# Optimization experiments

Hardware: AMD Instinct MI355X
Metric: run time of the kernel (lower is better)

The kernel has to match this reference:

```python
import jax, jax.numpy as jnp
import numpy as np

B, S, E, H = 16, 2048, 128, 128  # batch, seq_len, n_embd, head_dim


def setup_inputs() -> dict:
    key = jax.random.key(0)
    ks = jax.random.split(key, 6)
    init_s = 1.0 / np.sqrt(E)  # ~ torch Linear default init scale
    return {
        "q": jax.random.normal(ks[0], (B, S, E), jnp.float32),
        "k": jax.random.normal(ks[1], (B, S, E), jnp.float32),
        "v": jax.random.normal(ks[2], (B, S, E), jnp.float32),
        "Wq": jax.random.normal(ks[3], (H, E), jnp.float32) * init_s,
        "bq": jnp.zeros((H,), jnp.float32),
        "Wk": jax.random.normal(ks[4], (H, E), jnp.float32) * init_s,
        "bk": jnp.zeros((H,), jnp.float32),
        "Wv": jax.random.normal(ks[5], (H, E), jnp.float32) * init_s,
        "bv": jnp.zeros((H,), jnp.float32),
        "mask": jnp.tril(jnp.ones((S, S), jnp.float32)),  # causal mask
    }


def reference(q, k, v, Wq, bq, Wk, bk, Wv, bv, mask):
    # Linear projections: y = x @ W.T + b (torch nn.Linear convention)
    qh = q @ Wq.T + bq  # [B,S,H]
    kh = k @ Wk.T + bk  # [B,S,H]
    vh = v @ Wv.T + bv  # [B,S,H]
    d_k = kh.shape[-1]
    wei = jnp.einsum("bqd,bkd->bqk", qh, kh) * (d_k ** -0.5)  # [B,S,S]
    wei = jnp.where(mask == 0, -jnp.inf, wei)  # masked_fill(mask==0, -inf)
    attn = jax.nn.softmax(wei, axis=-1)
    return jnp.einsum("bqk,bkd->bqd", attn, vh)  # [B,S,H]
```

## Files before the change

### kernel.cpp

```cpp
#include <hip/hip_runtime.h>
#include <hip/hip_bf16.h>

#define BATCH 16
#define SEQ   2048
#define HD    128
#define TB    64
#define QB3   64
#define NT3   (SEQ/QB3)
#define PLANE ((size_t)BATCH*SEQ*HD)

typedef __attribute__((ext_vector_type(8))) short bf16x8;
typedef __attribute__((ext_vector_type(4))) float f32x4;
typedef __attribute__((ext_vector_type(2))) unsigned int u32x2;

#define MFMA(a,b,c) __builtin_amdgcn_mfma_f32_16x16x32_bf16(a,b,c,0,0,0)

__device__ __forceinline__ short f2bf(float f){
  union{float f; unsigned u;} v; v.f = f;
  unsigned r = (v.u + 0x7FFFu + ((v.u>>16)&1u))>>16;
  return (short)r;
}
__device__ __forceinline__ unsigned packbf(float lo, float hi){
  return ((unsigned)(unsigned short)f2bf(hi) << 16) | (unsigned short)f2bf(lo);
}
__device__ __forceinline__ bf16x8 pack8(f32x4 a, f32x4 b){
  bf16x8 r;
  r[0]=f2bf(a[0]); r[1]=f2bf(a[1]); r[2]=f2bf(a[2]); r[3]=f2bf(a[3]);
  r[4]=f2bf(b[0]); r[5]=f2bf(b[1]); r[6]=f2bf(b[2]); r[7]=f2bf(b[3]);
  return r;
}
__device__ __forceinline__ bf16x8 ldfrag(const float* base, size_t eo){
  const float* p = base + eo;
  return pack8(*(const f32x4*)p, *(const f32x4*)(p+4));
}

__global__ __launch_bounds__(256)
void wconv_kernel(const float* __restrict__ Wq, const float* __restrict__ Wk,
                  const float* __restrict__ Wv, short* __restrict__ wb)
{
  int i = (blockIdx.x*256 + threadIdx.x)*8;
  const float* src = (i < 16384) ? Wq : (i < 32768 ? Wk : Wv);
  int off = i & 16383;
  f32x4 a = *(const f32x4*)(src + off);
  f32x4 b = *(const f32x4*)(src + off + 4);
  *(bf16x8*)(wb + i) = pack8(a, b);
}

__global__ __launch_bounds__(256)
void proj_kernel(const float* __restrict__ k, const float* __restrict__ v,
                 const float* __restrict__ bk, const float* __restrict__ bv,
                 const short* __restrict__ wb, short* __restrict__ ws)
{
  __shared__ __align__(16) short T[TB*136];
  __shared__ __align__(16) short VT[HD*72];

  const int z = blockIdx.y + 1;
  const float* x  = (z==1) ? k  : v;
  const float* bb = (z==1) ? bk : bv;
  const short* W  = wb + (size_t)z*HD*HD;

  const int tid = threadIdx.x;
  const int w = tid>>6, l = tid&63, li = l&15, g = l>>4;
  const int bx = blockIdx.x;
  const int rowbase = bx*TB + w*16;

  bf16x8 afr[4];
  const float* xr = x + (size_t)(rowbase+li)*HD + g*8;
  #pragma unroll
  for (int ks=0; ks<4; ks++) afr[ks] = ldfrag(xr, (size_t)ks*32);

  f32x4 acc[8];
  #pragma unroll
  for (int ct=0; ct<8; ct++) acc[ct] = (f32x4){0.f,0.f,0.f,0.f};
  #pragma unroll
  for (int ct=0; ct<8; ct++){
    #pragma unroll
    for (int ks=0; ks<4; ks++){
      bf16x8 bfr = *(const bf16x8*)(W + (size_t)(ct*16+li)*HD + ks*32 + g*8);
      acc[ct] = MFMA(afr[ks], bfr, acc[ct]);
    }
  }

  const int img  = (bx>>1);
  const int half = bx & 1;

  if (z == 1){
    #pragma unroll
    for (int ct=0; ct<8; ct++){
      float bias = bb[ct*16+li];
      #pragma unroll
      for (int r=0; r<4; r++)
        T[(w*16+g*4+r)*136 + ct*16+li] = f2bf(acc[ct][r] + bias);
    }
    __syncthreads();
    short* dst = ws + PLANE + (size_t)img*16384;
    #pragma unroll
    for (int it=0; it<4; it++){
      int c = tid + it*256, row = c>>4, c8 = c&15;
      int r128 = half*64 + row;
      int chunk = r128*16 + (c8 ^ (r128&7));
      *(bf16x8*)(dst + chunk*8) = *(const bf16x8*)&T[row*136 + c8*8];
    }
  } else {
    #pragma unroll
    for (int ct=0; ct<8; ct++){
      float bias = bb[ct*16+li];
      #pragma unroll
      for (int r=0; r<4; r++)
        VT[(ct*16+li)*72 + w*16+g*4+r] = f2bf(acc[ct][r] + bias);
    }
    __syncthreads();
    short* dst = ws + 2*PLANE + (size_t)img*16384;
    const int d = tid>>1, hf = tid&1;
    #pragma unroll
    for (int j=0; j<4; j++){
      int c8l = hf*4 + j;
      int c8g = half*8 + c8l;
      int chunk = d*16 + (c8g ^ (d&7));
      *(bf16x8*)(dst + chunk*8) = *(const bf16x8*)&VT[d*72 + c8l*8];
    }
  }
}

__global__ __launch_bounds__(256, 2)
void attn_kernel(const float* __restrict__ qin, const float* __restrict__ bq,
                 const short* __restrict__ wb, const short* __restrict__ ws,
                 float* __restrict__ out)
{
  __shared__ __align__(16) short KVL[2][16384];
  __shared__ __align__(16) short PL[4][16*72];

  const int bid  = blockIdx.x;
  const int xcd  = bid & 7, slot = bid >> 3;
  const int b    = xcd*2 + (slot >> 5);
  const int sl   = slot & 31;
  const int qt   = (slot < 32) ? sl : (31 - sl);

  const int tid = threadIdx.x;
  const int w = tid>>6, l = tid&63, li = l&15, g = l>>4;

  const short* KimgB = ws + PLANE   + (size_t)b*(SEQ/128)*16384;
  const short* VimgB = ws + 2*PLANE + (size_t)b*(SEQ/128)*16384;

  const size_t qbase = (size_t)b*SEQ + qt*QB3;
  short* Pw = &PL[w][0];
  const float sc = 0.088388347648318447f;

  bf16x8 stg[8];
  #define LOADT(kt_) do{                                                     \
    const short* sK = KimgB + (size_t)((kt_)>>1)*16384 + ((kt_)&1)*8192;     \
    const short* sV = VimgB + (size_t)((kt_)>>1)*16384;                      \
    const int vh = ((kt_)&1)*8;                                              \
    _Pragma("unroll")                                                        \
    for (int j=0;j<4;j++) stg[j] = *(const bf16x8*)(sK + (tid + j*256)*8);   \
    _Pragma("unroll")                                                        \
    for (int j=0;j<4;j++){                                                   \
      int i = tid + j*256, d = i>>3, c8s = i&7;                              \
      stg[4+j] = *(const bf16x8*)(sV + (d*16 + vh + c8s)*8);                 \
    }                                                                        \
  }while(0)
  #define WRT(nb_) do{                                                      \
    short* dK = &KVL[nb_][0];                                               \
    short* dV = &KVL[nb_][8192];                                            \
    _Pragma("unroll")                                                       \
    for (int j=0;j<4;j++) *(bf16x8*)(dK + (tid+j*256)*8) = stg[j];          \
    _Pragma("unroll")                                                       \
    for (int j=0;j<4;j++) *(bf16x8*)(dV + (tid+j*256)*8) = stg[4+j];        \
  }while(0)

  LOADT(0);

  bf16x8 qfr[4];
  {
    bf16x8 xa[4];
    const float* xr = qin + (qbase + w*16 + li)*HD + g*8;
    #pragma unroll
    for (int ks=0; ks<4; ks++) xa[ks] = ldfrag(xr, (size_t)ks*32);
    f32x4 qa[8];
    #pragma unroll
    for (int ct=0; ct<8; ct++) qa[ct] = (f32x4){0.f,0.f,0.f,0.f};
    #pragma unroll
    for (int ct=0; ct<8; ct++){
      #pragma unroll
      for (int ks=0; ks<4; ks++){
        bf16x8 wf = *(const bf16x8*)(wb + (size_t)(ct*16+li)*HD + ks*32 + g*8);
        qa[ct] = MFMA(xa[ks], wf, qa[ct]);
      }
    }
    short* T = &KVL[0][0];
    #pragma unroll
    for (int ct=0; ct<8; ct++){
      float bias = bq[ct*16+li];
      #pragma unroll
      for (int r=0; r<4; r++)
        T[(w*16+g*4+r)*136 + ct*16+li] = f2bf(qa[ct][r] + bias);
    }
    __syncthreads();
    #pragma unroll
    for (int ks=0; ks<4; ks++)
      qfr[ks] = *(const bf16x8*)&T[(w*16+li)*136 + ks*32 + g*8];
    __syncthreads();
  }

  f32x4 oacc[8];
  #pragma unroll
  for (int dt=0; dt<8; dt++) oacc[dt] = (f32x4){0.f,0.f,0.f,0.f};
  float mreg = -1e30f, lreg = 0.f;

  WRT(0); __syncthreads();
  int cur = 0;

  for (int kt=0; kt<=qt; kt++){
    const bool pre = (kt < qt);
    if (pre) LOADT(kt+1);

    const short* KL = &KVL[cur][0];
    const short* VL = &KVL[cur][8192];

    f32x4 st[4];
    #pragma unroll
    for (int ct=0; ct<4; ct++) st[ct] = (f32x4){0.f,0.f,0.f,0.f};
    __builtin_amdgcn_s_setprio(1);
    #pragma unroll
    for (int ct=0; ct<4; ct++){
      const int row = ct*16 + li;
      #pragma unroll
      for (int ks=0; ks<4; ks++){
        const int chunk = row*16 + ((ks*4 + g) ^ (row&7));
        bf16x8 kfr = *(const bf16x8*)&KL[chunk*8];
        st[ct] = MFMA(kfr, qfr[ks], st[ct]);
      }
    }
    __builtin_amdgcn_s_setprio(0);

    float sv[4][4];
    float pm = -1e30f;
    const bool diag = (kt == qt);
    const int qloc = w*16 + li;
    #pragma unroll
    for (int ct=0; ct<4; ct++){
      #pragma unroll
      for (int r=0; r<4; r++){
        float x = st[ct][r]*sc;
        if (diag && (ct*16 + g*4 + r) > qloc) x = -1e30f;
        sv[ct][r] = x;
        pm = fmaxf(pm, x);
      }
    }
    pm = fmaxf(pm, __shfl_xor(pm, 16));
    pm = fmaxf(pm, __shfl_xor(pm, 32));
    const bool resc = !__all(pm - mreg <= 8.f);
    float sclq = 1.f;
    if (resc){
      float mn = fmaxf(mreg, pm);
      sclq = __expf(mreg - mn);
      mreg = mn;
      lreg *= sclq;
    }
    float psum = 0.f;
    #pragma unroll
    for (int ct=0; ct<4; ct++){
      #pragma unroll
      for (int r=0; r<4; r++){
        float p = __expf(sv[ct][r] - mreg);
        sv[ct][r] = p;
        psum += p;
      }
    }
    psum += __shfl_xor(psum, 16);
    psum += __shfl_xor(psum, 32);
    lreg += psum;

    #pragma unroll
    for (int c4=0; c4<4; c4++){
      u32x2 pw;
      pw[0] = packbf(sv[c4][0], sv[c4][1]);
      pw[1] = packbf(sv[c4][2], sv[c4][3]);
      *(u32x2*)&Pw[li*72 + c4*16 + g*4] = pw;
    }

    if (resc){
      float sclo[4];
      #pragma unroll
      for (int r=0; r<4; r++) sclo[r] = __shfl(sclq, g*4 + r);
      #pragma unroll
      for (int dt=0; dt<8; dt++){
        #pragma unroll
        for (int r=0; r<4; r++) oacc[dt][r] *= sclo[r];
      }
    }

    __builtin_amdgcn_s_setprio(1);
    #pragma unroll
    for (int ks2=0; ks2<2; ks2++){
      bf16x8 afr = *(const bf16x8*)&Pw[li*72 + ks2*32 + g*8];
      #pragma unroll
      for (int dt=0; dt<8; dt++){
        const int d = dt*16 + li;
        const int chunk = d*8 + ((ks2*4 + g) ^ (d&7));
        bf16x8 bfr = *(const bf16x8*)&VL[chunk*8];
        oacc[dt] = MFMA(afr, bfr, oacc[dt]);
      }
    }
    __builtin_amdgcn_s_setprio(0);

    if (pre) WRT(cur^1);
    __syncthreads();
    cur ^= 1;
  }

  float lso[4];
  #pragma unroll
  for (int r=0; r<4; r++) lso[r] = __shfl(lreg, g*4 + r);
  float* Ob = out + qbase*HD;
  #pragma unroll
  for (int dt=0; dt<8; dt++){
    #pragma unroll
    for (int r=0; r<4; r++){
      Ob[(size_t)(w*16 + g*4 + r)*HD + dt*16 + li] = oacc[dt][r] / lso[r];
    }
  }
  #undef LOADT
  #undef WRT
}

extern "C" void kernel_launch(void* const* d_in, const int* in_sizes, int n_in,
                              void* d_out, int out_size, void* d_ws, size_t ws_size,
                              hipStream_t stream)
{
  short* ws = (short*)d_ws;
  short* wb = ws + 3*PLANE;

  wconv_kernel<<<24, 256, 0, stream>>>(
      (const float*)d_in[3], (const float*)d_in[5], (const float*)d_in[7], wb);

  dim3 pg(BATCH*SEQ/TB, 2);
  proj_kernel<<<pg, 256, 0, stream>>>(
      (const float*)d_in[1], (const float*)d_in[2],
      (const float*)d_in[6], (const float*)d_in[8],
      wb, ws);

  attn_kernel<<<dim3(BATCH*NT3), 256, 0, stream>>>(
      (const float*)d_in[0], (const float*)d_in[4], wb, ws, (float*)d_out);
}
```

Measured before the change: 92.93 us.

## Split long causal query tiles across two blocks with split-KV merge

Query tiles 16-31 now have their key range split in half across two blocks, each writing bf16 partial outputs plus running max and sum to workspace. A new merge kernel combines the two halves with log-sum-exp rescaling. Tiles 0-15 still run in one block and write directly. The aim is to balance per-block work under causal masking and raise the block count from 512 to 768. The cost is an extra kernel launch, workspace traffic, and bf16 rounding of the partial outputs.

```diff
diff --git a/kernel.cpp b/kernel.cpp
--- a/kernel.cpp
+++ b/kernel.cpp
@@ -8,6 +8,8 @@
 #define QB3   64
 #define NT3   (SEQ/QB3)
 #define PLANE ((size_t)BATCH*SEQ*HD)
+#define WBOFF (3*PLANE)
+#define MLOFF (3*PLANE + 49152)
 
 typedef __attribute__((ext_vector_type(8))) short bf16x8;
 typedef __attribute__((ext_vector_type(4))) float f32x4;
@@ -19,6 +21,9 @@
   union{float f; unsigned u;} v; v.f = f;
   unsigned r = (v.u + 0x7FFFu + ((v.u>>16)&1u))>>16;
   return (short)r;
+}
+__device__ __forceinline__ float bf2f(short s){
+  union{unsigned u; float f;} v; v.u = ((unsigned)(unsigned short)s)<<16; return v.f;
 }
 __device__ __forceinline__ unsigned packbf(float lo, float hi){
   return ((unsigned)(unsigned short)f2bf(hi) << 16) | (unsigned short)f2bf(lo);
@@ -124,17 +129,35 @@
 
 __global__ __launch_bounds__(256, 2)
 void attn_kernel(const float* __restrict__ qin, const float* __restrict__ bq,
-                 const short* __restrict__ wb, const short* __restrict__ ws,
-                 float* __restrict__ out)
+                 short* __restrict__ ws, float* __restrict__ out)
 {
   __shared__ __align__(16) short KVL[2][16384];
   __shared__ __align__(16) short PL[4][16*72];
 
-  const int bid  = blockIdx.x;
-  const int xcd  = bid & 7, slot = bid >> 3;
-  const int b    = xcd*2 + (slot >> 5);
-  const int sl   = slot & 31;
-  const int qt   = (slot < 32) ? sl : (31 - sl);
+  const short* wb = ws + WBOFF;
+  const int bid = blockIdx.x;
+
+  int b, qt, kt0, kt1, pidx;
+  bool direct;
+  if (bid < 512){
+    const int xcd = bid & 7, r = bid >> 3;
+    b = xcd*2 + (r >> 5);
+    const int t = r & 31;
+    qt = 31 - (t >> 1);
+    const int h = t & 1;
+    const int sp = (qt + 1) >> 1;
+    kt0 = h ? sp : 0;
+    kt1 = h ? qt : sp - 1;
+    pidx = (b*16 + (qt - 16))*2 + h;
+    direct = false;
+  } else {
+    const int db = bid - 512;
+    const int xcd = db & 7, r2 = db >> 3;
+    b = xcd*2 + (r2 >> 4);
+    qt = 15 - (r2 & 15);
+    kt0 = 0; kt1 = qt; pidx = 0;
+    direct = true;
+  }
 
   const int tid = threadIdx.x;
   const int w = tid>>6, l = tid&63, li = l&15, g = l>>4;
@@ -168,7 +191,7 @@
     for (int j=0;j<4;j++) *(bf16x8*)(dV + (tid+j*256)*8) = stg[4+j];        \
   }while(0)
 
-  LOADT(0);
+  LOADT(kt0);
 
   bf16x8 qfr[4];
   {
@@ -210,8 +233,8 @@
   WRT(0); __syncthreads();
   int cur = 0;
 
-  for (int kt=0; kt<=qt; kt++){
-    const bool pre = (kt < qt);
+  for (int kt=kt0; kt<=kt1; kt++){
+    const bool pre = (kt < kt1);
     if (pre) LOADT(kt+1);
 
     const short* KL = &KVL[cur][0];
@@ -309,19 +332,72 @@
     cur ^= 1;
   }
 
-  float lso[4];
-  #pragma unroll
-  for (int r=0; r<4; r++) lso[r] = __shfl(lreg, g*4 + r);
-  float* Ob = out + qbase*HD;
-  #pragma unroll
-  for (int dt=0; dt<8; dt++){
-    #pragma unroll
-    for (int r=0; r<4; r++){
-      Ob[(size_t)(w*16 + g*4 + r)*HD + dt*16 + li] = oacc[dt][r] / lso[r];
+  if (direct){
+    float lso[4];
+    #pragma unroll
+    for (int r=0; r<4; r++) lso[r] = __shfl(lreg, g*4 + r);
+    float* Ob = out + qbase*HD;
+    #pragma unroll
+    for (int dt=0; dt<8; dt++){
+      #pragma unroll
+      for (int r=0; r<4; r++){
+        Ob[(size_t)(w*16 + g*4 + r)*HD + dt*16 + li] = oacc[dt][r] / lso[r];
+      }
+    }
+  } else {
+    short* Pp = ws + (size_t)pidx*8192;
+    #pragma unroll
+    for (int dt=0; dt<8; dt++){
+      #pragma unroll
+      for (int r=0; r<4; r++){
+        Pp[(w*16 + g*4 + r)*HD + dt*16 + li] = f2bf(oacc[dt][r]);
+      }
+    }
+    if (l < 16){
+      float* ml = (float*)(ws + MLOFF);
+      ml[pidx*128 + (w*16 + li)*2    ] = mreg;
+      ml[pidx*128 + (w*16 + li)*2 + 1] = lreg;
     }
   }
   #undef LOADT
   #undef WRT
+}
+
+__global__ __launch_bounds__(256)
+void merge_kernel(const short* __restrict__ ws, float* __restrict__ out)
+{
+  const int mb = blockIdx.x;
+  const int xcd = mb & 7, r3 = mb >> 3;
+  const int b  = xcd*2 + (r3 >> 4);
+  const int qt = 16 + (r3 & 15);
+
+  const int tid = threadIdx.x;
+  const int row = tid >> 2;
+  const int cg  = (tid & 3)*32;
+
+  const int p0 = (b*16 + (qt - 16))*2;
+  const short* P0 = ws + (size_t)p0*8192;
+  const short* P1 = ws + (size_t)(p0+1)*8192;
+  const float* ml = (const float*)(ws + MLOFF);
+
+  const float m0 = ml[p0*128 + row*2],     l0 = ml[p0*128 + row*2 + 1];
+  const float m1 = ml[(p0+1)*128 + row*2], l1 = ml[(p0+1)*128 + row*2 + 1];
+  const float M  = fmaxf(m0, m1);
+  const float w0 = __expf(m0 - M), w1 = __expf(m1 - M);
+  const float inv = 1.f / (l0*w0 + l1*w1);
+
+  float* Ob = out + ((size_t)b*SEQ + qt*QB3 + row)*HD + cg;
+  const short* a0 = P0 + row*HD + cg;
+  const short* a1 = P1 + row*HD + cg;
+  #pragma unroll
+  for (int j8=0; j8<4; j8++){
+    bf16x8 x0 = *(const bf16x8*)(a0 + j8*8);
+    bf16x8 x1 = *(const bf16x8*)(a1 + j8*8);
+    #pragma unroll
+    for (int e=0; e<8; e++){
+      Ob[j8*8 + e] = (bf2f(x0[e])*w0 + bf2f(x1[e])*w1) * inv;
+    }
+  }
 }
 
 extern "C" void kernel_launch(void* const* d_in, const int* in_sizes, int n_in,
@@ -329,7 +405,7 @@
                               hipStream_t stream)
 {
   short* ws = (short*)d_ws;
-  short* wb = ws + 3*PLANE;
+  short* wb = ws + WBOFF;
 
   wconv_kernel<<<24, 256, 0, stream>>>(
       (const float*)d_in[3], (const float*)d_in[5], (const float*)d_in[7], wb);
@@ -340,6 +416,8 @@
       (const float*)d_in[6], (const float*)d_in[8],
       wb, ws);
 
-  attn_kernel<<<dim3(BATCH*NT3), 256, 0, stream>>>(
-      (const float*)d_in[0], (const float*)d_in[4], wb, ws, (float*)d_out);
-}
+  attn_kernel<<<dim3(768), 256, 0, stream>>>(
+      (const float*)d_in[0], (const float*)d_in[4], ws, (float*)d_out);
+
+  merge_kernel<<<dim3(256), 256, 0, stream>>>(ws, (float*)d_out);
+}
```

New measurement: 106.0 us. 14.1% more time.
